# Performance work log

Measured on AMD Instinct MI355X. Metric: run time of the kernel, lower is better.

Reference implementation:

```python
import jax, jax.numpy as jnp
import numpy as np

B, S, D, H, E = 2, 1024, 1024, 4096, 8


def _xavier(key, shape):
    # matches torch.nn.init.xavier_uniform_ on a 3D tensor: fan_in/out from last two dims
    fan_in, fan_out = shape[-2], shape[-1]
    limit = float(np.sqrt(6.0 / (fan_in + fan_out)))
    return jax.random.uniform(key, shape, jnp.float32, -limit, limit)


def setup_inputs() -> dict:
    key = jax.random.key(0)
    ks = jax.random.split(key, 4)
    x = jax.random.normal(ks[0], (B, S, D), jnp.float32)
    router_w = jax.random.normal(ks[1], (D, E), jnp.float32) * (1.0 / np.sqrt(D))
    router_b = jnp.zeros((E,), jnp.float32)
    fc1_weight = _xavier(ks[2], (E, D, H))
    fc1_bias = jnp.zeros((E, H), jnp.float32)
    fc2_weight = _xavier(ks[3], (E, H, D))
    fc2_bias = jnp.zeros((E, D), jnp.float32)
    return {
        "x": x,
        "router_w": router_w,
        "router_b": router_b,
        "fc1_weight": fc1_weight,
        "fc1_bias": fc1_bias,
        "fc2_weight": fc2_weight,
        "fc2_bias": fc2_bias,
    }


def reference(x, router_w, router_b, fc1_weight, fc1_bias, fc2_weight, fc2_bias):
    b, s, d = x.shape
    x_flat = x.reshape(-1, d)                                  # [T, D]
    logits = x_flat @ router_w + router_b                       # [T, E]
    probs = jax.nn.softmax(logits, axis=-1)                     # [T, E]
    # per-expert FC1 + exact GELU (torch nn.GELU default is erf-based)
    h = jnp.einsum('td,edh->teh', x_flat, fc1_weight) + fc1_bias  # [T, E, H]
    h = jax.nn.gelu(h, approximate=False)
    expert_out = jnp.einsum('teh,ehd->ted', h, fc2_weight) + fc2_bias  # [T, E, D]
    out_flat = jnp.einsum('te,ted->td', probs, expert_out)      # [T, D]
    y = out_flat.reshape(b, s, d)
    router_probs = probs.reshape(b, s, -1)
    return y, router_probs
```

## Files before the change

### kernel.cpp

```cpp
#include <hip/hip_runtime.h>
#include <math.h>


typedef float f32x4 __attribute__((ext_vector_type(4)));
typedef __bf16 bf16x8 __attribute__((ext_vector_type(8)));
typedef __bf16 bf16x4 __attribute__((ext_vector_type(4)));

#define GLL16(gp, lp)                                                          \
  __builtin_amdgcn_global_load_lds(                                            \
      (const __attribute__((address_space(1))) void*)(gp),                     \
      (__attribute__((address_space(3))) void*)(lp), 16, 0, 0)

__device__ __forceinline__ float gelu_f(float h) {
  float x = h * 0.70710678118654752f;
  float ax = fabsf(x);
  float t = __builtin_amdgcn_rcpf(fmaf(0.3275911f, ax, 1.0f));
  float p = fmaf(1.061405429f, t, -1.453152027f);
  p = fmaf(p, t, 1.421413741f);
  p = fmaf(p, t, -0.284496736f);
  p = fmaf(p, t, 0.254829592f);
  float e = __expf(-x * x);
  float erfv = fmaf(-p * t, e, 1.0f);
  erfv = copysignf(erfv, x);
  return 0.5f * h * (1.0f + erfv);
}

__global__ void router_kernel(const float* __restrict__ x,
                              const float* __restrict__ rw,
                              const float* __restrict__ rb,
                              float* __restrict__ P,
                              float* __restrict__ probs_out)
{
  int gid = blockIdx.x * blockDim.x + threadIdx.x;
  int t = gid >> 6;
  int l = gid & 63;
  const float* xr = x + (size_t)t * 1024;
  float a[8];
#pragma unroll
  for (int e = 0; e < 8; ++e) a[e] = 0.f;
  for (int d = l; d < 1024; d += 64) {
    float xv = xr[d];
    f32x4 w0 = *(const f32x4*)(rw + d * 8);
    f32x4 w1 = *(const f32x4*)(rw + d * 8 + 4);
#pragma unroll
    for (int e = 0; e < 4; ++e) a[e] += xv * w0[e];
#pragma unroll
    for (int e = 0; e < 4; ++e) a[4 + e] += xv * w1[e];
  }
#pragma unroll
  for (int off = 32; off > 0; off >>= 1) {
#pragma unroll
    for (int e = 0; e < 8; ++e) a[e] += __shfl_down(a[e], off);
  }
  if (l == 0) {
#pragma unroll
    for (int e = 0; e < 8; ++e) a[e] += rb[e];
    float m = a[0];
#pragma unroll
    for (int e = 1; e < 8; ++e) m = fmaxf(m, a[e]);
    float s = 0.f;
#pragma unroll
    for (int e = 0; e < 8; ++e) { a[e] = __expf(a[e] - m); s += a[e]; }
    float inv = 1.f / s;
#pragma unroll
    for (int e = 0; e < 8; ++e) {
      float p = a[e] * inv;
      if (P) P[t * 8 + e] = p;
      probs_out[t * 8 + e] = p;
    }
  }
}

__global__ void cvt_kernel(const float* __restrict__ src,
                           __bf16* __restrict__ dst)
{
  size_t i = ((size_t)blockIdx.x * 256 + threadIdx.x) * 8;
  f32x4 v0 = *(const f32x4*)(src + i);
  f32x4 v1 = *(const f32x4*)(src + i + 4);
  bf16x8 o;
#pragma unroll
  for (int j = 0; j < 4; ++j) o[j] = (__bf16)v0[j];
#pragma unroll
  for (int j = 0; j < 4; ++j) o[4 + j] = (__bf16)v1[j];
  *(bf16x8*)(dst + i) = o;
}

__global__ void transconv_kernel(const float* __restrict__ src,
                                 __bf16* __restrict__ dst,
                                 int R, int C, int cChunk,
                                 size_t dstLd, size_t zOff)
{
  size_t bs = (size_t)blockIdx.z * (size_t)R * (size_t)C;
  size_t dzo = (size_t)blockIdx.z * zOff;
  int r0 = (blockIdx.x * 256 + threadIdx.x) * 4;
  int c0 = blockIdx.y * cChunk;
  const float* s = src + bs + (size_t)r0 * C;
  for (int c = c0; c < c0 + cChunk; c += 8) {
    float v[4][8];
#pragma unroll
    for (int rr = 0; rr < 4; ++rr) {
      f32x4 a = *(const f32x4*)(s + (size_t)rr * C + c);
      f32x4 b = *(const f32x4*)(s + (size_t)rr * C + c + 4);
#pragma unroll
      for (int j = 0; j < 4; ++j) { v[rr][j] = a[j]; v[rr][4 + j] = b[j]; }
    }
#pragma unroll
    for (int j = 0; j < 8; ++j) {
      bf16x4 o = {(__bf16)v[0][j], (__bf16)v[1][j], (__bf16)v[2][j],
                  (__bf16)v[3][j]};
      *(bf16x4*)(dst + (size_t)(c + j) * dstLd + dzo + r0) = o;
    }
  }
}

__device__ __forceinline__ void mfma_loop256(
    const char* Ab, const char* Bb, size_t ldaB, size_t ldbB, int K,
    char* lds, f32x4 acc[8][4])
{
  const int tid = threadIdx.x;
  const int w = tid >> 6, l = tid & 63;
  const int wm = w >> 2, wn = w & 3;
  const int m16 = l & 15, q = l >> 4;
  const int posB = ((q ^ ((m16 >> 1) & 3)) << 4);
  const int aE = (wm * 128 + m16) * 64 + posB;
  const int bE = 16384 + (wn * 64 + m16) * 64 + posB;
  const int sc16 = (((l & 3) ^ ((l >> 3) & 3)) << 4);
  const size_t sAoff = (size_t)(w * 32 + (l >> 2)) * ldaB + sc16;
  const size_t sBoff = (size_t)(w * 32 + (l >> 2)) * ldbB + sc16;
  const int ldst = w * 32 * 64;
  const int NT = K >> 5;

#define STAGE256(u)                                                            \
  {                                                                            \
    char* dA = lds + (((u) & 3) * 32768) + ldst;                               \
    const char* gA = Ab + sAoff + ((size_t)(u) << 6);                          \
    GLL16(gA, dA);                                                             \
    GLL16(gA + 16 * ldaB, dA + 1024);                                          \
    char* dB = dA + 16384;                                                     \
    const char* gB = Bb + sBoff + ((size_t)(u) << 6);                          \
    GLL16(gB, dB);                                                             \
    GLL16(gB + 16 * ldbB, dB + 1024);                                          \
  }

#define KFRAGS(T)                                                              \
    const char* ring = lds + (((T) & 3) * 32768);                              \
    bf16x8 bv[4], af[8];                                                       \
    _Pragma("unroll") for (int nj = 0; nj < 4; ++nj)                           \
        bv[nj] = *(const bf16x8*)(ring + bE + nj * 1024);                      \
    _Pragma("unroll") for (int mi = 0; mi < 8; ++mi)                           \
        af[mi] = *(const bf16x8*)(ring + aE + mi * 1024);

#define KMFMA                                                                  \
    __builtin_amdgcn_s_setprio(1);                                             \
    _Pragma("unroll") for (int mi = 0; mi < 8; ++mi)                           \
      _Pragma("unroll") for (int nj = 0; nj < 4; ++nj)                         \
        acc[mi][nj] = __builtin_amdgcn_mfma_f32_16x16x32_bf16(                 \
            af[mi], bv[nj], acc[mi][nj], 0, 0, 0);                             \
    __builtin_amdgcn_s_setprio(0);

#define KSYNC(n)                                                               \
    asm volatile("s_waitcnt vmcnt(" #n ") lgkmcnt(0)" ::: "memory");           \
    __builtin_amdgcn_s_barrier();

  STAGE256(0);
  STAGE256(1);
  STAGE256(2);
  KSYNC(8);

  int t = 0;
  for (; t < NT - 3; ++t) {
    KFRAGS(t);
    STAGE256(t + 3);
    KMFMA;
    KSYNC(8);
  }
  {
    KFRAGS(t);
    KMFMA;
    KSYNC(0);
  }
  ++t;
  {
    KFRAGS(t);
    KMFMA;
  }
  ++t;
  {
    KFRAGS(t);
    KMFMA;
  }
#undef STAGE256
#undef KFRAGS
#undef KMFMA
#undef KSYNC
}

__device__ __forceinline__ int xcd_swz(int id, int nwg) {
  return ((nwg & 7) == 0) ? ((id & 7) * (nwg >> 3) + (id >> 3)) : id;
}

__global__ __launch_bounds__(512, 2) void gemm1_kernel(
    const __bf16* __restrict__ X, const __bf16* __restrict__ W1T,
    const float* __restrict__ b1, const float* __restrict__ P,
    __bf16* __restrict__ Hs, int hs_ld, int e_off, size_t b_zstride)
{
  __shared__ __align__(16) char lds[131072];
  const int nwg = gridDim.x * gridDim.y * gridDim.z;
  const int id = blockIdx.x + gridDim.x * (blockIdx.y + gridDim.y * blockIdx.z);
  const int wg = xcd_swz(id, nwg);
  const int bm = wg & 7;
  const int bn = (wg >> 3) % gridDim.y;
  const int z = wg / (gridDim.y << 3);
  const int e = z + e_off;

  f32x4 acc[8][4];
  const f32x4 z4 = {0.f, 0.f, 0.f, 0.f};
#pragma unroll
  for (int i = 0; i < 8; ++i)
#pragma unroll
    for (int j = 0; j < 4; ++j) acc[i][j] = z4;

  const char* A = (const char*)(X + (size_t)bm * 256 * 1024);
  const char* B = (const char*)(W1T + (size_t)z * b_zstride +
                                (size_t)bn * 256 * 1024);
  mfma_loop256(A, B, 2048, 2048, 1024, lds, acc);

  const int tid = threadIdx.x, w = tid >> 6, l = tid & 63;
  const int wm = w >> 2, wn = w & 3, q = l >> 4, m16 = l & 15;
  const int row0 = bm * 256 + wm * 128 + q * 4;
  const int colE = bn * 256 + wn * 64 + m16;
  const int zcol = (hs_ld == 4096) ? 0 : z * 4096;
  float b1v[4];
#pragma unroll
  for (int nj = 0; nj < 4; ++nj)
    b1v[nj] = b1[(size_t)e * 4096 + colE + nj * 16];
#pragma unroll
  for (int mi = 0; mi < 8; ++mi) {
    float pv[4];
#pragma unroll
    for (int r = 0; r < 4; ++r)
      pv[r] = P[(size_t)(row0 + mi * 16 + r) * 8 + e];
#pragma unroll
    for (int nj = 0; nj < 4; ++nj)
#pragma unroll
      for (int r = 0; r < 4; ++r) {
        float h = acc[mi][nj][r] + b1v[nj];
        float o = gelu_f(h) * pv[r];
        Hs[(size_t)(row0 + mi * 16 + r) * hs_ld + zcol + colE + nj * 16] =
            (__bf16)o;
      }
  }
}

__global__ __launch_bounds__(512, 2) void gemm2_kernel(
    const __bf16* __restrict__ Hs, const __bf16* __restrict__ W2T,
    float* __restrict__ accb, int lda, int ldb, int kz, int Kb)
{
  __shared__ __align__(16) char lds[131072];
  const int nwg = gridDim.x * gridDim.y * gridDim.z;
  const int id = blockIdx.x + gridDim.x * (blockIdx.y + gridDim.y * blockIdx.z);
  const int wg = xcd_swz(id, nwg);
  const int bm = wg & 7;
  const int bn = (wg >> 3) % gridDim.y;
  const int z = wg / (gridDim.y << 3);

  f32x4 acc[8][4];
  const f32x4 z4 = {0.f, 0.f, 0.f, 0.f};
#pragma unroll
  for (int i = 0; i < 8; ++i)
#pragma unroll
    for (int j = 0; j < 4; ++j) acc[i][j] = z4;

  const char* A = (const char*)(Hs + (size_t)bm * 256 * lda + (size_t)z * kz);
  const char* B = (const char*)(W2T + (size_t)bn * 256 * ldb + (size_t)z * kz);
  mfma_loop256(A, B, (size_t)lda * 2, (size_t)ldb * 2, Kb, lds, acc);

  const int tid = threadIdx.x, w = tid >> 6, l = tid & 63;
  const int wm = w >> 2, wn = w & 3, q = l >> 4, m16 = l & 15;
  const int row0 = bm * 256 + wm * 128 + q * 4;
  const int col0 = bn * 256 + wn * 64 + m16;
#pragma unroll
  for (int mi = 0; mi < 8; ++mi)
#pragma unroll
    for (int nj = 0; nj < 4; ++nj)
#pragma unroll
      for (int r = 0; r < 4; ++r)
        unsafeAtomicAdd(
            accb + (size_t)(row0 + mi * 16 + r) * 1024 + col0 + nj * 16,
            acc[mi][nj][r]);
}

__global__ void finalize_kernel(const float* __restrict__ accb,
                                const float* __restrict__ P,
                                const float* __restrict__ b2,
                                float* __restrict__ y)
{
  int idx = blockIdx.x * 256 + threadIdx.x;
  int t = idx >> 8;
  int d0 = (idx & 255) << 2;
  f32x4 a = *(const f32x4*)(accb + (size_t)t * 1024 + d0);
#pragma unroll
  for (int e = 0; e < 8; ++e) {
    float p = P[t * 8 + e];
    f32x4 b = *(const f32x4*)(b2 + (size_t)e * 1024 + d0);
#pragma unroll
    for (int c = 0; c < 4; ++c) a[c] += p * b[c];
  }
  *(f32x4*)(y + (size_t)t * 1024 + d0) = a;
}

__global__ __launch_bounds__(256) void fused_naive_kernel(
    const float* __restrict__ x, const float* __restrict__ w1,
    const float* __restrict__ b1, const float* __restrict__ w2,
    const float* __restrict__ b2, const float* __restrict__ probs,
    float* __restrict__ y)
{
  __shared__ float xs[8][1024];
  __shared__ float gs[8][64];
  __shared__ float ps[8];
  const int tid = threadIdx.x;
  const int t0 = blockIdx.x * 8;
  const size_t DH = (size_t)1024 * 4096;
  const int tt = tid >> 5;
  const int d0 = (tid & 31) * 32;
  float acc[32];
#pragma unroll
  for (int i = 0; i < 32; ++i) acc[i] = 0.f;
  {
    const f32x4* xsrc = (const f32x4*)(x + (size_t)t0 * 1024);
    f32x4* xdst = (f32x4*)&xs[0][0];
    for (int i = tid; i < 2048; i += 256) xdst[i] = xsrc[i];
  }
  const int wv = tid >> 6;
  const int hl = tid & 63;
  for (int e = 0; e < 8; ++e) {
    if (tid < 8) ps[tid] = probs[(size_t)(t0 + tid) * 8 + e];
    __syncthreads();
    for (int hc = 0; hc < 4096; hc += 64) {
      float a0 = 0.f, a1 = 0.f;
      const float* w1p = w1 + (size_t)e * DH + hc + hl;
      for (int d = 0; d < 1024; ++d) {
        float wvv = w1p[(size_t)d * 4096];
        a0 += xs[wv * 2 + 0][d] * wvv;
        a1 += xs[wv * 2 + 1][d] * wvv;
      }
      __syncthreads();
      gs[wv * 2 + 0][hl] =
          ps[wv * 2 + 0] * gelu_f(a0 + b1[(size_t)e * 4096 + hc + hl]);
      gs[wv * 2 + 1][hl] =
          ps[wv * 2 + 1] * gelu_f(a1 + b1[(size_t)e * 4096 + hc + hl]);
      __syncthreads();
      const float* w2p = w2 + (size_t)e * DH + (size_t)hc * 1024 + d0;
      for (int hh = 0; hh < 64; ++hh) {
        float g = gs[tt][hh];
#pragma unroll
        for (int jb = 0; jb < 8; ++jb) {
          f32x4 w4 = *(const f32x4*)(w2p + (size_t)hh * 1024 + jb * 4);
#pragma unroll
          for (int j2 = 0; j2 < 4; ++j2) acc[jb * 4 + j2] += g * w4[j2];
        }
      }
    }
#pragma unroll
    for (int j = 0; j < 32; ++j)
      acc[j] += ps[tt] * b2[(size_t)e * 1024 + d0 + j];
    __syncthreads();
  }
  float* yp = y + (size_t)(t0 + tt) * 1024 + d0;
#pragma unroll
  for (int jb = 0; jb < 8; ++jb) {
    f32x4 o = {acc[jb * 4], acc[jb * 4 + 1], acc[jb * 4 + 2], acc[jb * 4 + 3]};
    *(f32x4*)(yp + jb * 4) = o;
  }
}

extern "C" void kernel_launch(void* const* d_in, const int* in_sizes, int n_in,
                              void* d_out, int out_size, void* d_ws,
                              size_t ws_size, hipStream_t stream)
{
  const float* x  = (const float*)d_in[0];
  const float* rw = (const float*)d_in[1];
  const float* rb = (const float*)d_in[2];
  const float* w1 = (const float*)d_in[3];
  const float* b1 = (const float*)d_in[4];
  const float* w2 = (const float*)d_in[5];
  const float* b2 = (const float*)d_in[6];
  float* y = (float*)d_out;
  float* probs_out = y + (size_t)2048 * 1024;

  const size_t DH = (size_t)1024 * 4096;
  const size_t BASE = (64 << 10) + (size_t)2048 * 1024 * 4 +
                      (size_t)2048 * 1024 * 2;
  const size_t TA = BASE + 8 * DH * 2 + (size_t)2048 * 32768 * 2;
  const size_t TB = BASE + DH * 2 + (size_t)2048 * 4096 * 2;

  char* ws = (char*)d_ws;
  float* P = (float*)ws;
  float* accb = (float*)(ws + (64 << 10));
  __bf16* xb = (__bf16*)(ws + (64 << 10) + (size_t)2048 * 1024 * 4);
  char* ws2 = ws + BASE;

  if (ws_size >= TA) {
    router_kernel<<<512, 256, 0, stream>>>(x, rw, rb, P, probs_out);
    hipMemsetAsync(accb, 0, (size_t)2048 * 1024 * 4, stream);
    cvt_kernel<<<1024, 256, 0, stream>>>(x, xb);
    __bf16* WT = (__bf16*)ws2;
    __bf16* Hs = WT + 8 * DH;
    transconv_kernel<<<dim3(1, 64, 8), 256, 0, stream>>>(
        w1, WT, 1024, 4096, 64, 1024, DH);
    gemm1_kernel<<<dim3(8, 16, 8), 512, 0, stream>>>(xb, WT, b1, P, Hs,
                                                     32768, 0, DH);
    transconv_kernel<<<dim3(4, 16, 8), 256, 0, stream>>>(
        w2, WT, 4096, 1024, 64, 32768, 4096);
    gemm2_kernel<<<dim3(8, 4, 8), 512, 0, stream>>>(Hs, WT, accb, 32768,
                                                    32768, 4096, 4096);
    finalize_kernel<<<2048, 256, 0, stream>>>(accb, P, b2, y);
  } else if (ws_size >= TB) {
    router_kernel<<<512, 256, 0, stream>>>(x, rw, rb, P, probs_out);
    hipMemsetAsync(accb, 0, (size_t)2048 * 1024 * 4, stream);
    cvt_kernel<<<1024, 256, 0, stream>>>(x, xb);
    __bf16* WT = (__bf16*)ws2;
    __bf16* HsE = WT + DH;
    for (int e = 0; e < 8; ++e) {
      transconv_kernel<<<dim3(1, 64, 1), 256, 0, stream>>>(
          w1 + e * DH, WT, 1024, 4096, 64, 1024, 0);
      gemm1_kernel<<<dim3(8, 16, 1), 512, 0, stream>>>(xb, WT, b1, P, HsE,
                                                       4096, e, 0);
      transconv_kernel<<<dim3(4, 16, 1), 256, 0, stream>>>(
          w2 + e * DH, WT, 4096, 1024, 64, 4096, 0);
      gemm2_kernel<<<dim3(8, 4, 4), 512, 0, stream>>>(HsE, WT, accb, 4096,
                                                      4096, 1024, 1024);
    }
    finalize_kernel<<<2048, 256, 0, stream>>>(accb, P, b2, y);
  } else {
    router_kernel<<<512, 256, 0, stream>>>(x, rw, rb, (float*)nullptr,
                                           probs_out);
    fused_naive_kernel<<<256, 256, 0, stream>>>(x, w1, b1, w2, b2, probs_out,
                                                y);
  }
}
```

Baseline: 728.8 us.

## Restructure GEMM mainloop to 64-wide K double buffer and tile weight transpose

The shared 256x256 MFMA mainloop moves from a 4-deep ring of 32-wide K tiles to a 2-deep double buffer of 64-wide K tiles. It uses an XOR swizzle over 8 chunks and splits each K step into four quarter-tile MFMA phases, with the next tile's global-to-LDS loads interleaved between barriers. The weight transpose-convert kernel becomes a 64x64 LDS-tiled transpose with coalesced reads and 16-byte bf16 writes, and runs on a much larger grid. The aim is better load/compute overlap and higher transpose bandwidth. The price is many extra barriers per K step and a shallower prefetch depth.

```diff
diff --git a/kernel.cpp b/kernel.cpp
--- a/kernel.cpp
+++ b/kernel.cpp
@@ -4,7 +4,6 @@
 
 typedef float f32x4 __attribute__((ext_vector_type(4)));
 typedef __bf16 bf16x8 __attribute__((ext_vector_type(8)));
-typedef __bf16 bf16x4 __attribute__((ext_vector_type(4)));
 
 #define GLL16(gp, lp)                                                          \
   __builtin_amdgcn_global_load_lds(                                            \
@@ -87,29 +86,30 @@
 
 __global__ void transconv_kernel(const float* __restrict__ src,
                                  __bf16* __restrict__ dst,
-                                 int R, int C, int cChunk,
-                                 size_t dstLd, size_t zOff)
-{
+                                 int R, int C, size_t dstLd, size_t zOff)
+{
+  __shared__ float tile[64][65];
   size_t bs = (size_t)blockIdx.z * (size_t)R * (size_t)C;
   size_t dzo = (size_t)blockIdx.z * zOff;
-  int r0 = (blockIdx.x * 256 + threadIdx.x) * 4;
-  int c0 = blockIdx.y * cChunk;
-  const float* s = src + bs + (size_t)r0 * C;
-  for (int c = c0; c < c0 + cChunk; c += 8) {
-    float v[4][8];
-#pragma unroll
-    for (int rr = 0; rr < 4; ++rr) {
-      f32x4 a = *(const f32x4*)(s + (size_t)rr * C + c);
-      f32x4 b = *(const f32x4*)(s + (size_t)rr * C + c + 4);
-#pragma unroll
-      for (int j = 0; j < 4; ++j) { v[rr][j] = a[j]; v[rr][4 + j] = b[j]; }
-    }
-#pragma unroll
-    for (int j = 0; j < 8; ++j) {
-      bf16x4 o = {(__bf16)v[0][j], (__bf16)v[1][j], (__bf16)v[2][j],
-                  (__bf16)v[3][j]};
-      *(bf16x4*)(dst + (size_t)(c + j) * dstLd + dzo + r0) = o;
-    }
+  int r0 = blockIdx.x * 64, c0 = blockIdx.y * 64;
+  int tr = threadIdx.x >> 4;
+  int tc = (threadIdx.x & 15) * 4;
+#pragma unroll
+  for (int i = 0; i < 4; ++i) {
+    f32x4 v = *(const f32x4*)(src + bs + (size_t)(r0 + tr + 16 * i) * C + c0 + tc);
+#pragma unroll
+    for (int j = 0; j < 4; ++j) tile[tr + 16 * i][tc + j] = v[j];
+  }
+  __syncthreads();
+  int oc = threadIdx.x >> 3;
+  int orr = (threadIdx.x & 7) * 8;
+#pragma unroll
+  for (int i = 0; i < 2; ++i) {
+    int c = oc + 32 * i;
+    bf16x8 o;
+#pragma unroll
+    for (int j = 0; j < 8; ++j) o[j] = (__bf16)tile[orr + j][c];
+    *(bf16x8*)(dst + (size_t)(c0 + c) * dstLd + dzo + r0 + orr) = o;
   }
 }
 
@@ -121,78 +121,106 @@
   const int w = tid >> 6, l = tid & 63;
   const int wm = w >> 2, wn = w & 3;
   const int m16 = l & 15, q = l >> 4;
-  const int posB = ((q ^ ((m16 >> 1) & 3)) << 4);
-  const int aE = (wm * 128 + m16) * 64 + posB;
-  const int bE = 16384 + (wn * 64 + m16) * 64 + posB;
-  const int sc16 = (((l & 3) ^ ((l >> 3) & 3)) << 4);
-  const size_t sAoff = (size_t)(w * 32 + (l >> 2)) * ldaB + sc16;
-  const size_t sBoff = (size_t)(w * 32 + (l >> 2)) * ldbB + sc16;
-  const int ldst = w * 32 * 64;
-  const int NT = K >> 5;
-
-#define STAGE256(u)                                                            \
+  const int swz = m16 & 7;
+  const int aBase = wm * 16384 + m16 * 128;
+  const int bBase = 32768 + (wn >> 1) * 16384 + ((wn & 1) * 64 + m16) * 128;
+  const int srcCh = ((l & 7) ^ ((l >> 3) & 7)) << 4;
+  const size_t gA0 = (size_t)(w * 16 + (l >> 3)) * ldaB + srcCh;
+  const size_t gB0 = (size_t)(w * 16 + (l >> 3)) * ldbB + srcCh;
+  const int dstW = w * 2048;
+  const int NT = K >> 6;
+
+  bf16x8 af[4][2], bv[4][2];
+
+#define STG_A(h, tau)                                                          \
   {                                                                            \
-    char* dA = lds + (((u) & 3) * 32768) + ldst;                               \
-    const char* gA = Ab + sAoff + ((size_t)(u) << 6);                          \
-    GLL16(gA, dA);                                                             \
-    GLL16(gA + 16 * ldaB, dA + 1024);                                          \
-    char* dB = dA + 16384;                                                     \
-    const char* gB = Bb + sBoff + ((size_t)(u) << 6);                          \
-    GLL16(gB, dB);                                                             \
-    GLL16(gB + 16 * ldbB, dB + 1024);                                          \
-  }
-
-#define KFRAGS(T)                                                              \
-    const char* ring = lds + (((T) & 3) * 32768);                              \
-    bf16x8 bv[4], af[8];                                                       \
-    _Pragma("unroll") for (int nj = 0; nj < 4; ++nj)                           \
-        bv[nj] = *(const bf16x8*)(ring + bE + nj * 1024);                      \
-    _Pragma("unroll") for (int mi = 0; mi < 8; ++mi)                           \
-        af[mi] = *(const bf16x8*)(ring + aE + mi * 1024);
-
-#define KMFMA                                                                  \
-    __builtin_amdgcn_s_setprio(1);                                             \
-    _Pragma("unroll") for (int mi = 0; mi < 8; ++mi)                           \
-      _Pragma("unroll") for (int nj = 0; nj < 4; ++nj)                         \
-        acc[mi][nj] = __builtin_amdgcn_mfma_f32_16x16x32_bf16(                 \
-            af[mi], bv[nj], acc[mi][nj], 0, 0, 0);                             \
-    __builtin_amdgcn_s_setprio(0);
-
-#define KSYNC(n)                                                               \
-    asm volatile("s_waitcnt vmcnt(" #n ") lgkmcnt(0)" ::: "memory");           \
-    __builtin_amdgcn_s_barrier();
-
-  STAGE256(0);
-  STAGE256(1);
-  STAGE256(2);
-  KSYNC(8);
+    char* d = lds + (((tau) & 1) * 65536) + (h) * 16384 + dstW;                \
+    const char* g = Ab + gA0 + (size_t)((h) * 128) * ldaB + (size_t)(tau) * 128;\
+    GLL16(g, d);                                                               \
+    GLL16(g + 8 * ldaB, d + 1024);                                             \
+  }
+#define STG_B(h, tau)                                                          \
+  {                                                                            \
+    char* d = lds + (((tau) & 1) * 65536) + 32768 + (h) * 16384 + dstW;        \
+    const char* g = Bb + gB0 + (size_t)((h) * 128) * ldbB + (size_t)(tau) * 128;\
+    GLL16(g, d);                                                               \
+    GLL16(g + 8 * ldbB, d + 1024);                                             \
+  }
+#define RD_A(lo, p)                                                            \
+  _Pragma("unroll") for (int mi = 0; mi < 4; ++mi)                             \
+  _Pragma("unroll") for (int ks = 0; ks < 2; ++ks)                             \
+    af[mi][ks] = *(const bf16x8*)(lds + (p) * 65536 + aBase +                  \
+        ((lo) * 4 + mi) * 2048 + (((ks * 4 + q) ^ swz) << 4));
+#define RD_B(no, p)                                                            \
+  _Pragma("unroll") for (int nj = 0; nj < 2; ++nj)                             \
+  _Pragma("unroll") for (int ks = 0; ks < 2; ++ks)                             \
+    bv[(no) * 2 + nj][ks] = *(const bf16x8*)(lds + (p) * 65536 + bBase +       \
+        ((no) * 2 + nj) * 2048 + (((ks * 4 + q) ^ swz) << 4));
+#define MM(lo, no)                                                             \
+  __builtin_amdgcn_s_setprio(1);                                               \
+  _Pragma("unroll") for (int mi = 0; mi < 4; ++mi)                             \
+  _Pragma("unroll") for (int nj = 0; nj < 2; ++nj)                             \
+  _Pragma("unroll") for (int ks = 0; ks < 2; ++ks)                             \
+    acc[(lo) * 4 + mi][(no) * 2 + nj] =                                        \
+        __builtin_amdgcn_mfma_f32_16x16x32_bf16(                               \
+            af[mi][ks], bv[(no) * 2 + nj][ks],                                 \
+            acc[(lo) * 4 + mi][(no) * 2 + nj], 0, 0, 0);                       \
+  __builtin_amdgcn_s_setprio(0);
+#define SB __builtin_amdgcn_sched_barrier(0)
+#define BAR { SB; __builtin_amdgcn_s_barrier(); SB; }
+#define VMW(n) asm volatile("s_waitcnt vmcnt(" #n ")" ::: "memory")
+
+  STG_A(0, 0); STG_A(1, 0); STG_B(0, 0); STG_B(1, 0);
+  STG_B(0, 1); STG_B(1, 1);
+  VMW(4);
+  BAR;
 
   int t = 0;
-  for (; t < NT - 3; ++t) {
-    KFRAGS(t);
-    STAGE256(t + 3);
-    KMFMA;
-    KSYNC(8);
+  for (; t < NT - 2; ++t) {
+    const int p = t & 1;
+    RD_A(0, p); RD_B(0, p);
+    STG_A(0, t + 1);
+    BAR; MM(0, 0); BAR;
+    RD_B(1, p);
+    STG_A(1, t + 1);
+    BAR; MM(0, 1); BAR;
+    RD_A(1, p);
+    STG_B(0, t + 2);
+    BAR; MM(1, 0); BAR;
+    STG_B(1, t + 2);
+    BAR; MM(1, 1); SB; VMW(4); BAR;
   }
   {
-    KFRAGS(t);
-    KMFMA;
-    KSYNC(0);
-  }
-  ++t;
+    const int p = t & 1;
+    RD_A(0, p); RD_B(0, p);
+    STG_A(0, t + 1);
+    BAR; MM(0, 0); BAR;
+    RD_B(1, p);
+    STG_A(1, t + 1);
+    BAR; MM(0, 1); BAR;
+    RD_A(1, p);
+    BAR; MM(1, 0); BAR;
+    BAR; MM(1, 1); SB; VMW(0); BAR;
+    ++t;
+  }
   {
-    KFRAGS(t);
-    KMFMA;
-  }
-  ++t;
-  {
-    KFRAGS(t);
-    KMFMA;
-  }
-#undef STAGE256
-#undef KFRAGS
-#undef KMFMA
-#undef KSYNC
+    const int p = t & 1;
+    RD_A(0, p); RD_B(0, p);
+    MM(0, 0);
+    RD_B(1, p);
+    MM(0, 1);
+    RD_A(1, p);
+    MM(1, 0);
+    MM(1, 1);
+  }
+#undef STG_A
+#undef STG_B
+#undef RD_A
+#undef RD_B
+#undef MM
+#undef SB
+#undef BAR
+#undef VMW
 }
 
 __device__ __forceinline__ int xcd_swz(int id, int nwg) {
@@ -406,12 +434,12 @@
     cvt_kernel<<<1024, 256, 0, stream>>>(x, xb);
     __bf16* WT = (__bf16*)ws2;
     __bf16* Hs = WT + 8 * DH;
-    transconv_kernel<<<dim3(1, 64, 8), 256, 0, stream>>>(
-        w1, WT, 1024, 4096, 64, 1024, DH);
+    transconv_kernel<<<dim3(16, 64, 8), 256, 0, stream>>>(
+        w1, WT, 1024, 4096, 1024, DH);
     gemm1_kernel<<<dim3(8, 16, 8), 512, 0, stream>>>(xb, WT, b1, P, Hs,
                                                      32768, 0, DH);
-    transconv_kernel<<<dim3(4, 16, 8), 256, 0, stream>>>(
-        w2, WT, 4096, 1024, 64, 32768, 4096);
+    transconv_kernel<<<dim3(64, 16, 8), 256, 0, stream>>>(
+        w2, WT, 4096, 1024, 32768, 4096);
     gemm2_kernel<<<dim3(8, 4, 8), 512, 0, stream>>>(Hs, WT, accb, 32768,
                                                     32768, 4096, 4096);
     finalize_kernel<<<2048, 256, 0, stream>>>(accb, P, b2, y);
@@ -422,12 +450,12 @@
     __bf16* WT = (__bf16*)ws2;
     __bf16* HsE = WT + DH;
     for (int e = 0; e < 8; ++e) {
-      transconv_kernel<<<dim3(1, 64, 1), 256, 0, stream>>>(
-          w1 + e * DH, WT, 1024, 4096, 64, 1024, 0);
+      transconv_kernel<<<dim3(16, 64, 1), 256, 0, stream>>>(
+          w1 + e * DH, WT, 1024, 4096, 1024, 0);
       gemm1_kernel<<<dim3(8, 16, 1), 512, 0, stream>>>(xb, WT, b1, P, HsE,
                                                        4096, e, 0);
-      transconv_kernel<<<dim3(4, 16, 1), 256, 0, stream>>>(
-          w2 + e * DH, WT, 4096, 1024, 64, 4096, 0);
+      transconv_kernel<<<dim3(64, 16, 1), 256, 0, stream>>>(
+          w2 + e * DH, WT, 4096, 1024, 4096, 0);
       gemm2_kernel<<<dim3(8, 4, 4), 512, 0, stream>>>(HsE, WT, accb, 4096,
                                                       4096, 1024, 1024);
     }
```

New measurement: 620.0 us. 1.18x faster.
